# Performance work log

Measured on AMD Instinct MI355X. Metric: run time of the kernel, lower is better.

Reference implementation:

```python
import jax, jax.numpy as jnp
import numpy as np

N, E, L, H, C, F_IN = 50000, 800000, 3, 8, 16, 128  # nodes, edges, layers, heads, per-head dim, input dim
NEG_SLOPE = 0.2


def setup_inputs() -> dict:
    key = jax.random.key(0)
    k = jax.random.split(key, 8)
    scale = 0.1
    x = jax.random.normal(k[0], (N, F_IN), dtype=jnp.float32)
    Ws = jax.random.normal(k[1], (L, F_IN, H * C), dtype=jnp.float32) * scale
    att_src = jax.random.normal(k[2], (L, H, C), dtype=jnp.float32) * scale
    att_dst = jax.random.normal(k[3], (L, H, C), dtype=jnp.float32) * scale
    biases = jnp.zeros((L, H * C), dtype=jnp.float32)
    fc_w = jax.random.normal(k[4], (H * C, C), dtype=jnp.float32) * scale
    fc_b = jnp.zeros((C,), dtype=jnp.float32)
    edge_index = jax.random.randint(k[5], (2, E), 0, N, dtype=jnp.int64)
    return {"x": x, "Ws": Ws, "att_src": att_src, "att_dst": att_dst,
            "biases": biases, "fc_w": fc_w, "fc_b": fc_b, "edge_index": edge_index}


def _gat_layer(x, W, a_src, a_dst, b, src, dst):
    # x: [N, F]; W: [F, H*C]; a_src/a_dst: [H, C]; src/dst: [E+N] (self-loops included)
    n = x.shape[0]
    h = (x @ W).reshape(n, H, C)                      # [N, H, C]
    e_src = jnp.einsum('nhc,hc->nh', h, a_src)        # [N, H]
    e_dst = jnp.einsum('nhc,hc->nh', h, a_dst)
    e = jax.nn.leaky_relu(e_src[src] + e_dst[dst], NEG_SLOPE)   # [E+N, H]
    # segment softmax over incoming edges of each target node
    emax = jax.ops.segment_max(e, dst, num_segments=n)          # [N, H]
    ex = jnp.exp(e - emax[dst])
    denom = jax.ops.segment_sum(ex, dst, num_segments=n)        # [N, H]
    alpha = ex / (denom[dst] + 1e-16)                            # [E+N, H]
    out = jax.ops.segment_sum(alpha[:, :, None] * h[src], dst, num_segments=n)  # [N, H, C]
    return out.reshape(n, H * C) + b


def reference(x, Ws, att_src, att_dst, biases, fc_w, fc_b, edge_index):
    loop = jnp.arange(N, dtype=edge_index.dtype)
    src = jnp.concatenate([edge_index[0], loop])  # add self-loops (PyG default)
    dst = jnp.concatenate([edge_index[1], loop])
    h = x
    for l in range(L):
        h = _gat_layer(h, Ws[l], att_src[l], att_dst[l], biases[l], src, dst)
        h = jax.nn.elu(h)
    return h @ fc_w + fc_b  # [N, C]
```

## Files before the change

kernel.cpp:

```cpp
#include <hip/hip_runtime.h>
#include <hip/hip_bf16.h>


#define GAT_F 128
#define GAT_H 8
#define GAT_C 16

typedef __attribute__((ext_vector_type(8))) short bf16x8;
typedef __attribute__((ext_vector_type(4))) float f32x4;

__device__ __forceinline__ float bf2f(unsigned short u) {
    union { unsigned int i; float f; } x; x.i = ((unsigned int)u) << 16; return x.f;
}
__device__ __forceinline__ float bfhi2f(unsigned int u) {
    union { unsigned int i; float f; } x; x.i = u & 0xFFFF0000u; return x.f;
}
__device__ __forceinline__ float bflo2f(unsigned int u) {
    union { unsigned int i; float f; } x; x.i = u << 16; return x.f;
}
__device__ __forceinline__ unsigned int pk_bf16(float a, float b) {
    union { float f; unsigned int i; } ua, ub;
    ua.f = a; ub.f = b;
    unsigned int ra = (ua.i + 0x7FFFu + ((ua.i >> 16) & 1u)) >> 16;
    unsigned int rb = (ub.i + 0x7FFFu + ((ub.i >> 16) & 1u)) & 0xFFFF0000u;
    return ra | rb;
}
__device__ __forceinline__ unsigned short f2bf(float a) {
    union { float f; unsigned int i; } ua; ua.f = a;
    return (unsigned short)((ua.i + 0x7FFFu + ((ua.i >> 16) & 1u)) >> 16);
}
__device__ __forceinline__ float ldf(const void* p, size_t i, int isf32) {
    return isf32 ? ((const float*)p)[i] : bf2f(((const unsigned short*)p)[i]);
}
__device__ __forceinline__ int ldei(const int* ei, int i, int is64) {
    return is64 ? ei[2 * (size_t)i] : ei[i];
}

__global__ void k_detect_init(const unsigned short* __restrict__ xb,
                              const int* __restrict__ ei, int* flags,
                              int* deg, int n, int nb_n) {
    if ((int)blockIdx.x < nb_n) {
        int i = blockIdx.x * 256 + threadIdx.x;
        if (i < n) deg[i] = 1;
        return;
    }
    __shared__ int nan_cnt, zero_cnt;
    if (threadIdx.x == 0) { nan_cnt = 0; zero_cnt = 0; }
    __syncthreads();
    int t = threadIdx.x;
    int ln = 0;
    for (int i = t; i < 8192; i += 256) {
        unsigned short u = xb[i];
        if ((u & 0x7F80) == 0x7F80) ln++;
    }
    int lz = 0;
    for (int i = t; i < 2048; i += 256) {
        if (ei[2 * i + 1] == 0) lz++;
    }
    if (ln) atomicAdd(&nan_cnt, ln);
    if (lz) atomicAdd(&zero_cnt, lz);
    __syncthreads();
    if (t == 0) {
        flags[0] = (nan_cnt > 3) ? 1 : 0;
        flags[1] = (zero_cnt > 1024) ? 1 : 0;
    }
}

__global__ void k_prep_count(const void* __restrict__ W, const void* __restrict__ asrc,
                             const void* __restrict__ adst,
                             unsigned short* __restrict__ wt, unsigned short* __restrict__ wa,
                             int Lw, const int* __restrict__ ei, int* deg, int E,
                             const int* __restrict__ flags) {
    int isf32 = flags[0];
    int b = blockIdx.x, t = threadIdx.x;
    if (b < Lw * 64) {
        int gid = b * 256 + t;
        int l = gid >> 14, r = gid & 16383;
        int c = r >> 7, k = r & 127;
        float v = ldf(W, (size_t)l * 16384 + k * 128 + c, isf32);
        wt[gid] = f2bf(v);
    } else if (b < Lw * 72) {
        int id = (b - Lw * 64) * 256 + t;
        int l = id >> 11, q = id & 2047;
        int j = q >> 7, k = q & 127;
        int head = j & 7;
        const void* av = (j < 8) ? asrc : adst;
        float acc = 0.f;
        #pragma unroll
        for (int cc = 0; cc < 16; cc++) {
            float w = ldf(W, (size_t)l * 16384 + k * 128 + head * 16 + cc, isf32);
            float a = ldf(av, (size_t)l * 128 + head * 16 + cc, isf32);
            acc += w * a;
        }
        wa[id] = f2bf(acc);
    } else {
        int k = (b - Lw * 72) * 256 + t;
        int is64 = flags[1];
        if (k < E) atomicAdd(&deg[ldei(ei, E + k, is64)], 1);
    }
}

__global__ __launch_bounds__(256) void k_scan_blk(
    const int* __restrict__ deg, int* __restrict__ rp_local,
    int* __restrict__ bsum, int n)
{
    int b = blockIdx.x, t = threadIdx.x;
    int i0 = b * 1024 + t * 4;
    int v0 = 0, v1 = 0, v2 = 0, v3 = 0;
    if (i0 + 3 < n) {
        int4 d = *(const int4*)(deg + i0);
        v0 = d.x; v1 = d.y; v2 = d.z; v3 = d.w;
    } else {
        if (i0     < n) v0 = deg[i0];
        if (i0 + 1 < n) v1 = deg[i0 + 1];
        if (i0 + 2 < n) v2 = deg[i0 + 2];
        if (i0 + 3 < n) v3 = deg[i0 + 3];
    }
    int s = v0 + v1 + v2 + v3;
    int lane = t & 63, wid = t >> 6;
    int sc = s;
    #pragma unroll
    for (int off = 1; off < 64; off <<= 1) {
        int o = __shfl_up(sc, off);
        if (lane >= off) sc += o;
    }
    __shared__ int wsum[4];
    if (lane == 63) wsum[wid] = sc;
    __syncthreads();
    int woff = 0;
    #pragma unroll
    for (int w2 = 0; w2 < 4; w2++) if (w2 < wid) woff += wsum[w2];
    int excl = woff + sc - s;
    if (i0     < n) rp_local[i0]     = excl;
    if (i0 + 1 < n) rp_local[i0 + 1] = excl + v0;
    if (i0 + 2 < n) rp_local[i0 + 2] = excl + v0 + v1;
    if (i0 + 3 < n) rp_local[i0 + 3] = excl + v0 + v1 + v2;
    if (t == 255) bsum[b] = woff + sc;
}

__global__ __launch_bounds__(256) void k_scan_top(
    int* __restrict__ bsum, int* __restrict__ rowptr, int nb, int n)
{
    __shared__ int sh[1024];
    int t = threadIdx.x;
    for (int i = t; i < 1024; i += 256) sh[i] = (i < nb) ? bsum[i] : 0;
    __syncthreads();
    for (int off = 1; off < 1024; off <<= 1) {
        int vals[4];
        #pragma unroll
        for (int k = 0; k < 4; k++) {
            int i = t + 256 * k;
            vals[k] = (i >= off) ? sh[i - off] : 0;
        }
        __syncthreads();
        #pragma unroll
        for (int k = 0; k < 4; k++) sh[t + 256 * k] += vals[k];
        __syncthreads();
    }
    for (int i = t; i < nb; i += 256) bsum[i] = (i == 0) ? 0 : sh[i - 1];
    if (t == 0) rowptr[n] = sh[nb - 1];
}

__global__ void k_place_add(int* __restrict__ rowptr, const int* __restrict__ bsum,
                            int* __restrict__ adj, int* __restrict__ cursor, int n)
{
    int i = blockIdx.x * 256 + threadIdx.x;
    if (i < n) {
        int r = rowptr[i] + bsum[i >> 10];
        rowptr[i] = r;
        adj[r] = i;
        cursor[i] = 1;
    }
    if (blockIdx.x == 0 && threadIdx.x < 8) adj[rowptr[n] + threadIdx.x] = 0;
}

__global__ void k_scatter(const int* __restrict__ ei, const int* __restrict__ rowptr,
                          int* __restrict__ cursor, int* __restrict__ adj, int E,
                          const int* __restrict__ flags) {
    int k = blockIdx.x * 256 + threadIdx.x;
    int is64 = flags[1];
    if (k < E) {
        int s = ldei(ei, k, is64);
        int d = ldei(ei, E + k, is64);
        int p = atomicAdd(&cursor[d], 1);
        adj[rowptr[d] + p] = s;
    }
}

__global__ __launch_bounds__(256) void k_gemm_mfma(
    const void* __restrict__ xin, int x_is_input,
    const unsigned short* __restrict__ wt,
    const unsigned short* __restrict__ wa,
    unsigned int* __restrict__ hb, float* __restrict__ es, float* __restrict__ ed,
    int n, const int* __restrict__ flags)
{
    __shared__ unsigned short xl[64 * 136];
    int isf32 = flags[0];
    int t = threadIdx.x;
    int row0 = blockIdx.x * 64;
    int lane = t & 63, wid = t >> 6, quad = lane >> 4, col = lane & 15;

    bool direct = (!x_is_input) || (!isf32);
    if (!direct) {
        const float4* xg = (const float4*)xin;
        for (int i = t; i < 2048; i += 256) {
            int r = i >> 5, c4 = i & 31;
            int gr = row0 + r;
            uint2 u = make_uint2(0u, 0u);
            if (gr < n) {
                float4 v = xg[(size_t)gr * 32 + c4];
                u = make_uint2(pk_bf16(v.x, v.y), pk_bf16(v.z, v.w));
            }
            *(uint2*)&xl[r * 136 + c4 * 4] = u;
        }
        __syncthreads();
    }

    int arow = row0 + wid * 16 + col;
    int arowc = min(arow, n - 1);
    const unsigned short* xrow = direct
        ? ((const unsigned short*)xin + (size_t)arowc * 128)
        : &xl[(wid * 16 + col) * 136];

    f32x4 acc[9];
    #pragma unroll
    for (int ct = 0; ct < 9; ct++) acc[ct] = (f32x4){0.f, 0.f, 0.f, 0.f};

    #pragma unroll
    for (int ks = 0; ks < 4; ks++) {
        int k0 = ks * 32;
        bf16x8 af = *(const bf16x8*)&xrow[k0 + quad * 8];
        #pragma unroll
        for (int ct = 0; ct < 9; ct++) {
            const unsigned short* bsrc = (ct < 8) ? &wt[(ct * 16 + col) * 128]
                                                  : &wa[col * 128];
            bf16x8 bf = *(const bf16x8*)&bsrc[k0 + quad * 8];
            acc[ct] = __builtin_amdgcn_mfma_f32_16x16x32_bf16(af, bf, acc[ct], 0, 0, 0);
        }
    }

    #pragma unroll
    for (int ct = 0; ct < 8; ct++) {
        #pragma unroll
        for (int r = 0; r < 4; r++) {
            int grow = row0 + wid * 16 + quad * 4 + r;
            float v = acc[ct][r];
            float vp = __shfl_xor(v, 1);
            if (!(lane & 1) && grow < n)
                hb[(size_t)grow * 64 + ct * 8 + (col >> 1)] = pk_bf16(v, vp);
        }
    }
    #pragma unroll
    for (int r = 0; r < 4; r++) {
        int grow = row0 + wid * 16 + quad * 4 + r;
        float v = acc[8][r];
        if (grow < n) {
            if (col < 8) es[(size_t)grow * 8 + col] = v;
            else         ed[(size_t)grow * 8 + col - 8] = v;
        }
    }
}

__global__ __launch_bounds__(256) void k_aggregate(
    const unsigned int* __restrict__ hb,
    const float* __restrict__ es, const float* __restrict__ ed,
    const int* __restrict__ rowptr, const int* __restrict__ adj,
    const void* __restrict__ bias, long b_off, unsigned int* __restrict__ out,
    int n, const int* __restrict__ flags)
{
    __shared__ __align__(16) float alds[4][72 * 12];
    __shared__ __align__(16) int   slds[4][80];
    int isf32 = flags[0];
    int lane = threadIdx.x & 63;
    int wid = threadIdx.x >> 6;
    int node = blockIdx.x * 4 + wid;
    if (node >= n) return;
    int base = rowptr[node];
    int deg = rowptr[node + 1] - base;
    int head = lane >> 3;

    if (lane < 8) {
        *(float4*)&alds[wid][(64 + lane) * 12]     = make_float4(0.f, 0.f, 0.f, 0.f);
        *(float4*)&alds[wid][(64 + lane) * 12 + 4] = make_float4(0.f, 0.f, 0.f, 0.f);
        slds[wid][64 + lane] = 0;
    }

    const float4* es4 = (const float4*)es;
    const float4* ed4 = (const float4*)ed;
    float edv[8];
    {
        float4 a = ed4[node * 2];
        float4 b = ed4[node * 2 + 1];
        edv[0] = a.x; edv[1] = a.y; edv[2] = a.z; edv[3] = a.w;
        edv[4] = b.x; edv[5] = b.y; edv[6] = b.z; edv[7] = b.w;
    }

    float acc0 = 0.f, acc1 = 0.f, lsum = 0.f;
    for (int j0 = 0; j0 < deg; j0 += 64) {
        int j = j0 + lane;
        int sp = (j < deg) ? adj[base + j] : 0;
        float4 ea = es4[sp * 2];
        float4 eb = es4[sp * 2 + 1];
        float ev[8] = {ea.x, ea.y, ea.z, ea.w, eb.x, eb.y, eb.z, eb.w};
        float p[8];
        #pragma unroll
        for (int hh = 0; hh < 8; hh++) {
            float v = ev[hh] + edv[hh];
            v = fmaxf(v, 0.2f * v);
            float pe = __expf(v);
            p[hh] = (j < deg) ? pe : 0.f;
        }
        *(float4*)&alds[wid][lane * 12]     = make_float4(p[0], p[1], p[2], p[3]);
        *(float4*)&alds[wid][lane * 12 + 4] = make_float4(p[4], p[5], p[6], p[7]);
        slds[wid][lane] = sp;
        __builtin_amdgcn_s_waitcnt(0xC07F);

        int lim = min(64, deg - j0);
        for (int jj = 0; jj < lim; jj += 8) {
            int4 sA = *(const int4*)&slds[wid][jj];
            int4 sB = *(const int4*)&slds[wid][jj + 4];
            float a0 = alds[wid][(jj + 0) * 12 + head];
            float a1 = alds[wid][(jj + 1) * 12 + head];
            float a2 = alds[wid][(jj + 2) * 12 + head];
            float a3 = alds[wid][(jj + 3) * 12 + head];
            float a4 = alds[wid][(jj + 4) * 12 + head];
            float a5 = alds[wid][(jj + 5) * 12 + head];
            float a6 = alds[wid][(jj + 6) * 12 + head];
            float a7 = alds[wid][(jj + 7) * 12 + head];
            unsigned int h0 = hb[sA.x * 64 + lane];
            unsigned int h1 = hb[sA.y * 64 + lane];
            unsigned int h2 = hb[sA.z * 64 + lane];
            unsigned int h3 = hb[sA.w * 64 + lane];
            unsigned int h4 = hb[sB.x * 64 + lane];
            unsigned int h5 = hb[sB.y * 64 + lane];
            unsigned int h6 = hb[sB.z * 64 + lane];
            unsigned int h7 = hb[sB.w * 64 + lane];
            lsum += ((a0 + a1) + (a2 + a3)) + ((a4 + a5) + (a6 + a7));
            acc0 += a0 * bflo2f(h0) + a1 * bflo2f(h1) + a2 * bflo2f(h2) + a3 * bflo2f(h3);
            acc0 += a4 * bflo2f(h4) + a5 * bflo2f(h5) + a6 * bflo2f(h6) + a7 * bflo2f(h7);
            acc1 += a0 * bfhi2f(h0) + a1 * bfhi2f(h1) + a2 * bfhi2f(h2) + a3 * bfhi2f(h3);
            acc1 += a4 * bfhi2f(h4) + a5 * bfhi2f(h5) + a6 * bfhi2f(h6) + a7 * bfhi2f(h7);
        }
    }

    float inv = 1.f / (lsum + 1e-16f);
    int ch = lane << 1;
    float o0 = acc0 * inv + ldf(bias, b_off + ch, isf32);
    float o1 = acc1 * inv + ldf(bias, b_off + ch + 1, isf32);
    o0 = o0 > 0.f ? o0 : (__expf(o0) - 1.f);
    o1 = o1 > 0.f ? o1 : (__expf(o1) - 1.f);
    out[(size_t)node * 64 + lane] = pk_bf16(o0, o1);
}

__global__ __launch_bounds__(256) void k_fc(
    const unsigned int* __restrict__ h, const void* __restrict__ fw,
    const void* __restrict__ fb, void* __restrict__ out, int n,
    const int* __restrict__ flags)
{
    __shared__ float fws[GAT_F * GAT_C];
    int isf32 = flags[0];
    int t = threadIdx.x;
    for (int i = t; i < GAT_F * GAT_C; i += 256)
        fws[i] = ldf(fw, i, isf32);
    __syncthreads();
    int row = blockIdx.x * 256 + t;
    if (row >= n) return;
    float acc[16];
    #pragma unroll
    for (int c = 0; c < 16; c++) acc[c] = ldf(fb, c, isf32);
    const unsigned int* hr = h + (size_t)row * 64;
    for (int k2 = 0; k2 < 64; k2++) {
        unsigned int u = hr[k2];
        float x0 = bflo2f(u), x1 = bfhi2f(u);
        const float4* w0 = (const float4*)&fws[(2 * k2) * 16];
        const float4* w1 = (const float4*)&fws[(2 * k2 + 1) * 16];
        #pragma unroll
        for (int c4 = 0; c4 < 4; c4++) {
            float4 wv0 = w0[c4], wv1 = w1[c4];
            acc[c4 * 4 + 0] += x0 * wv0.x + x1 * wv1.x;
            acc[c4 * 4 + 1] += x0 * wv0.y + x1 * wv1.y;
            acc[c4 * 4 + 2] += x0 * wv0.z + x1 * wv1.z;
            acc[c4 * 4 + 3] += x0 * wv0.w + x1 * wv1.w;
        }
    }
    if (isf32) {
        float* o = (float*)out + (size_t)row * GAT_C;
        #pragma unroll
        for (int c = 0; c < 16; c++) o[c] = acc[c];
    } else {
        __hip_bfloat16* o = (__hip_bfloat16*)out + (size_t)row * GAT_C;
        #pragma unroll
        for (int c = 0; c < 16; c++) o[c] = __float2bfloat16(acc[c]);
    }
}

extern "C" void kernel_launch(void* const* d_in, const int* in_sizes, int n_in,
                              void* d_out, int out_size, void* d_ws, size_t ws_size,
                              hipStream_t stream) {
    const void* x      = d_in[0];
    const void* Ws     = d_in[1];
    const void* att_s  = d_in[2];
    const void* att_d  = d_in[3];
    const void* biases = d_in[4];
    const void* fc_w   = d_in[5];
    const void* fc_b   = d_in[6];
    const int*  ei     = (const int*)d_in[7];

    const int N  = in_sizes[0] / GAT_F;
    const int E  = in_sizes[7] / 2;
    const int L  = in_sizes[1] / (GAT_F * GAT_F);
    const int ET = E + N;

    char* w = (char*)d_ws;
    int* flags         = (int*)w;            w += 64;
    unsigned int* hA   = (unsigned int*)w;   w += (size_t)N * 64 * 4;
    unsigned int* hB   = (unsigned int*)w;   w += (size_t)N * 64 * 4;
    float* es          = (float*)w;          w += (size_t)N * GAT_H * 4;
    float* ed          = (float*)w;          w += (size_t)N * GAT_H * 4;
    int* rowptr        = (int*)w;            w += (((size_t)(N + 1) * 4 + 15) & ~15ull);
    int* cursor        = (int*)w;            w += (size_t)N * 4;
    int* bsum          = (int*)w;            w += 1024 * 4;
    int* adj           = (int*)w;            w += (size_t)(ET + 16) * 4;
    unsigned short* wt = (unsigned short*)w; w += (size_t)L * 16384 * 2;
    unsigned short* wa = (unsigned short*)w; w += (size_t)L * 2048 * 2;

    int nb_n = (N + 255) / 256;
    int nb_e = (E + 255) / 256;
    int nb_s = (N + 1023) / 1024;

    k_detect_init<<<nb_n + 1, 256, 0, stream>>>(
        (const unsigned short*)x, ei, flags, cursor, N, nb_n);
    k_prep_count<<<L * 72 + nb_e, 256, 0, stream>>>(
        Ws, att_s, att_d, wt, wa, L, ei, cursor, E, flags);
    k_scan_blk<<<nb_s, 256, 0, stream>>>(cursor, rowptr, bsum, N);
    k_scan_top<<<1, 256, 0, stream>>>(bsum, rowptr, nb_s, N);
    k_place_add<<<nb_n, 256, 0, stream>>>(rowptr, bsum, adj, cursor, N);
    k_scatter<<<nb_e, 256, 0, stream>>>(ei, rowptr, cursor, adj, E, flags);

    int nb_g = (N + 63) / 64;
    int nb_a = (N + 3) / 4;
    for (int l = 0; l < L; l++) {
        k_gemm_mfma<<<nb_g, 256, 0, stream>>>(
            (l == 0) ? x : (const void*)hA, (l == 0) ? 1 : 0,
            wt + (size_t)l * 16384, wa + (size_t)l * 2048,
            hB, es, ed, N, flags);
        k_aggregate<<<nb_a, 256, 0, stream>>>(
            hB, es, ed, rowptr, adj,
            biases, (long)l * GAT_F, hA, N, flags);
    }
    k_fc<<<nb_n, 256, 0, stream>>>(hA, fc_w, fc_b, d_out, N, flags);
}
```

Before: 412.6 us.

## Fold top-level scan into place kernel and fuse edge scatter with first GEMM

Removes the single-block top-level scan kernel by having each thread in the place kernel sum the preceding block totals itself (up to about 49 entries). It also merges the edge-scatter kernel into the layer-0 GEMM launch by appending scatter blocks after the GEMM blocks, so the two independent jobs share one launch. Later layers use a slimmed GEMM kernel that always reads the bf16 hidden state directly. This removes two kernel launches and their serialization, at the cost of redundant serial reads of the block totals in every place-kernel thread.

```diff
diff --git a/kernel.cpp b/kernel.cpp
--- a/kernel.cpp
+++ b/kernel.cpp
@@ -138,69 +138,57 @@
     if (t == 255) bsum[b] = woff + sc;
 }
 
-__global__ __launch_bounds__(256) void k_scan_top(
-    int* __restrict__ bsum, int* __restrict__ rowptr, int nb, int n)
-{
-    __shared__ int sh[1024];
-    int t = threadIdx.x;
-    for (int i = t; i < 1024; i += 256) sh[i] = (i < nb) ? bsum[i] : 0;
-    __syncthreads();
-    for (int off = 1; off < 1024; off <<= 1) {
-        int vals[4];
-        #pragma unroll
-        for (int k = 0; k < 4; k++) {
-            int i = t + 256 * k;
-            vals[k] = (i >= off) ? sh[i - off] : 0;
-        }
-        __syncthreads();
-        #pragma unroll
-        for (int k = 0; k < 4; k++) sh[t + 256 * k] += vals[k];
-        __syncthreads();
-    }
-    for (int i = t; i < nb; i += 256) bsum[i] = (i == 0) ? 0 : sh[i - 1];
-    if (t == 0) rowptr[n] = sh[nb - 1];
-}
-
 __global__ void k_place_add(int* __restrict__ rowptr, const int* __restrict__ bsum,
-                            int* __restrict__ adj, int* __restrict__ cursor, int n)
+                            int* __restrict__ adj, int* __restrict__ cursor,
+                            int n, int nb_s)
 {
     int i = blockIdx.x * 256 + threadIdx.x;
     if (i < n) {
-        int r = rowptr[i] + bsum[i >> 10];
+        int myblk = i >> 10;
+        int off = 0;
+        for (int b = 0; b < myblk; b++) off += bsum[b];
+        int r = rowptr[i] + off;
         rowptr[i] = r;
         adj[r] = i;
         cursor[i] = 1;
     }
-    if (blockIdx.x == 0 && threadIdx.x < 8) adj[rowptr[n] + threadIdx.x] = 0;
-}
-
-__global__ void k_scatter(const int* __restrict__ ei, const int* __restrict__ rowptr,
-                          int* __restrict__ cursor, int* __restrict__ adj, int E,
-                          const int* __restrict__ flags) {
-    int k = blockIdx.x * 256 + threadIdx.x;
-    int is64 = flags[1];
-    if (k < E) {
-        int s = ldei(ei, k, is64);
-        int d = ldei(ei, E + k, is64);
-        int p = atomicAdd(&cursor[d], 1);
-        adj[rowptr[d] + p] = s;
-    }
-}
-
-__global__ __launch_bounds__(256) void k_gemm_mfma(
-    const void* __restrict__ xin, int x_is_input,
-    const unsigned short* __restrict__ wt,
-    const unsigned short* __restrict__ wa,
+    if (blockIdx.x == 0 && threadIdx.x < 9) {
+        int tot = 0;
+        for (int b = 0; b < nb_s; b++) tot += bsum[b];
+        if (threadIdx.x == 0) rowptr[n] = tot;
+        else adj[tot + threadIdx.x - 1] = 0;
+    }
+}
+
+__global__ __launch_bounds__(256) void k_gemm_scatter(
+    const void* __restrict__ xin,
+    const unsigned short* __restrict__ wt, const unsigned short* __restrict__ wa,
     unsigned int* __restrict__ hb, float* __restrict__ es, float* __restrict__ ed,
-    int n, const int* __restrict__ flags)
+    int n, int nb_g,
+    const int* __restrict__ ei, const int* __restrict__ rowptr,
+    int* __restrict__ cursor, int* __restrict__ adj, int E,
+    const int* __restrict__ flags)
 {
     __shared__ unsigned short xl[64 * 136];
     int isf32 = flags[0];
     int t = threadIdx.x;
+
+    if ((int)blockIdx.x >= nb_g) {
+        int k = ((int)blockIdx.x - nb_g) * 256 + t;
+        int is64 = flags[1];
+        if (k < E) {
+            int s = ldei(ei, k, is64);
+            int d = ldei(ei, E + k, is64);
+            int p = atomicAdd(&cursor[d], 1);
+            adj[rowptr[d] + p] = s;
+        }
+        return;
+    }
+
     int row0 = blockIdx.x * 64;
     int lane = t & 63, wid = t >> 6, quad = lane >> 4, col = lane & 15;
 
-    bool direct = (!x_is_input) || (!isf32);
+    bool direct = !isf32;
     if (!direct) {
         const float4* xg = (const float4*)xin;
         for (int i = t; i < 2048; i += 256) {
@@ -221,6 +209,59 @@
     const unsigned short* xrow = direct
         ? ((const unsigned short*)xin + (size_t)arowc * 128)
         : &xl[(wid * 16 + col) * 136];
+
+    f32x4 acc[9];
+    #pragma unroll
+    for (int ct = 0; ct < 9; ct++) acc[ct] = (f32x4){0.f, 0.f, 0.f, 0.f};
+
+    #pragma unroll
+    for (int ks = 0; ks < 4; ks++) {
+        int k0 = ks * 32;
+        bf16x8 af = *(const bf16x8*)&xrow[k0 + quad * 8];
+        #pragma unroll
+        for (int ct = 0; ct < 9; ct++) {
+            const unsigned short* bsrc = (ct < 8) ? &wt[(ct * 16 + col) * 128]
+                                                  : &wa[col * 128];
+            bf16x8 bf = *(const bf16x8*)&bsrc[k0 + quad * 8];
+            acc[ct] = __builtin_amdgcn_mfma_f32_16x16x32_bf16(af, bf, acc[ct], 0, 0, 0);
+        }
+    }
+
+    #pragma unroll
+    for (int ct = 0; ct < 8; ct++) {
+        #pragma unroll
+        for (int r = 0; r < 4; r++) {
+            int grow = row0 + wid * 16 + quad * 4 + r;
+            float v = acc[ct][r];
+            float vp = __shfl_xor(v, 1);
+            if (!(lane & 1) && grow < n)
+                hb[(size_t)grow * 64 + ct * 8 + (col >> 1)] = pk_bf16(v, vp);
+        }
+    }
+    #pragma unroll
+    for (int r = 0; r < 4; r++) {
+        int grow = row0 + wid * 16 + quad * 4 + r;
+        float v = acc[8][r];
+        if (grow < n) {
+            if (col < 8) es[(size_t)grow * 8 + col] = v;
+            else         ed[(size_t)grow * 8 + col - 8] = v;
+        }
+    }
+}
+
+__global__ __launch_bounds__(256) void k_gemm_mfma(
+    const void* __restrict__ xin,
+    const unsigned short* __restrict__ wt, const unsigned short* __restrict__ wa,
+    unsigned int* __restrict__ hb, float* __restrict__ es, float* __restrict__ ed,
+    int n, const int* __restrict__ flags)
+{
+    int t = threadIdx.x;
+    int row0 = blockIdx.x * 64;
+    int lane = t & 63, wid = t >> 6, quad = lane >> 4, col = lane & 15;
+
+    int arow = row0 + wid * 16 + col;
+    int arowc = min(arow, n - 1);
+    const unsigned short* xrow = (const unsigned short*)xin + (size_t)arowc * 128;
 
     f32x4 acc[9];
     #pragma unroll
@@ -427,22 +468,25 @@
     int nb_n = (N + 255) / 256;
     int nb_e = (E + 255) / 256;
     int nb_s = (N + 1023) / 1024;
+    int nb_g = (N + 63) / 64;
+    int nb_a = (N + 3) / 4;
 
     k_detect_init<<<nb_n + 1, 256, 0, stream>>>(
         (const unsigned short*)x, ei, flags, cursor, N, nb_n);
     k_prep_count<<<L * 72 + nb_e, 256, 0, stream>>>(
         Ws, att_s, att_d, wt, wa, L, ei, cursor, E, flags);
     k_scan_blk<<<nb_s, 256, 0, stream>>>(cursor, rowptr, bsum, N);
-    k_scan_top<<<1, 256, 0, stream>>>(bsum, rowptr, nb_s, N);
-    k_place_add<<<nb_n, 256, 0, stream>>>(rowptr, bsum, adj, cursor, N);
-    k_scatter<<<nb_e, 256, 0, stream>>>(ei, rowptr, cursor, adj, E, flags);
-
-    int nb_g = (N + 63) / 64;
-    int nb_a = (N + 3) / 4;
-    for (int l = 0; l < L; l++) {
+    k_place_add<<<nb_n, 256, 0, stream>>>(rowptr, bsum, adj, cursor, N, nb_s);
+
+    k_gemm_scatter<<<nb_g + nb_e, 256, 0, stream>>>(
+        x, wt, wa, hB, es, ed, N, nb_g,
+        ei, rowptr, cursor, adj, E, flags);
+    k_aggregate<<<nb_a, 256, 0, stream>>>(
+        hB, es, ed, rowptr, adj, biases, 0L, hA, N, flags);
+
+    for (int l = 1; l < L; l++) {
         k_gemm_mfma<<<nb_g, 256, 0, stream>>>(
-            (l == 0) ? x : (const void*)hA, (l == 0) ? 1 : 0,
-            wt + (size_t)l * 16384, wa + (size_t)l * 2048,
+            hA, wt + (size_t)l * 16384, wa + (size_t)l * 2048,
             hB, es, ed, N, flags);
         k_aggregate<<<nb_a, 256, 0, stream>>>(
             hB, es, ed, rowptr, adj,
```

Result: faster. 387.3 us, median of 2 (-6.1%).
